# Optimization experiments

Hardware: AMD Instinct MI355X
Metric: run time of the kernel (lower is better)

The kernel has to match this reference:

```python
import jax, jax.numpy as jnp
import numpy as np

LATENT = 128
K_SUBTREES = 64      # children of the root '&&'
DEPTH = 11           # perfect binary subtree depth -> 2**11 = 2048 leaves each
N_NODES = 50000      # program-graph node embedding rows
N_TOKENS = 32        # len(LIST_PREDICATES) + len(LIST_OP)


def setup_inputs() -> dict:
    key = jax.random.key(0)
    ks = jax.random.split(key, 16)
    L = LATENT
    s = 0.08  # keep tanh/sigmoid out of saturation, like trained weights
    return {
        "node_embedding": jax.random.normal(ks[0], (N_NODES, L), jnp.float32) * 0.5,
        "init_embedding": jax.random.normal(ks[1], (1, L), jnp.float32) * 0.5,
        "char_embedding": jax.random.normal(ks[2], (N_TOKENS, L), jnp.float32) * 0.5,
        # stacked gate weights, y = x @ W + b
        # W_child order: ilh, irh, lflh, lfrh, rflh, rfrh, ulh, urh
        "W_child": jax.random.normal(ks[3], (8, L, L), jnp.float32) * s,
        "b_child": jax.random.normal(ks[4], (8, L), jnp.float32) * s,
        # W_x order: ix, fx, ux
        "W_x": jax.random.normal(ks[5], (3, L, L), jnp.float32) * s,
        "b_x": jax.random.normal(ks[6], (3, L), jnp.float32) * s,
        # W_leaf order: cx, ox
        "W_leaf": jax.random.normal(ks[7], (2, L, L), jnp.float32) * s,
        "b_leaf": jax.random.normal(ks[8], (2, L), jnp.float32) * s,
        # W_and order: and_transform_c, and_transform_h
        "W_and": jax.random.normal(ks[9], (2, L, L), jnp.float32) * s,
        "b_and": jax.random.normal(ks[10], (2, L), jnp.float32) * s,
        "W_oend": jax.random.normal(ks[11], (3 * L, L), jnp.float32) * s,
        "b_oend": jax.random.normal(ks[12], (L,), jnp.float32) * s,
        "leaf_idx": jax.random.randint(ks[13], (K_SUBTREES, 2 ** DEPTH), 0, N_NODES, jnp.int32),
        "op_idx": jax.random.randint(ks[14], (K_SUBTREES, 2 ** DEPTH - 1), 0, N_TOKENS, jnp.int32),
    }


def reference(node_embedding, init_embedding, char_embedding,
              W_child, b_child, W_x, b_x, W_leaf, b_leaf,
              W_and, b_and, W_oend, b_oend, leaf_idx, op_idx):
    n_leaves = leaf_idx.shape[1]
    depth = int(np.log2(n_leaves))

    # --- leaves: c = cx(x); h = sigmoid(ox(x)) * tanh(c) ---
    x = node_embedding[leaf_idx]                      # [K, M, L]
    c = x @ W_leaf[0] + b_leaf[0]
    h = jax.nn.sigmoid(x @ W_leaf[1] + b_leaf[1]) * jnp.tanh(c)

    # --- internal binary Tree-LSTM cells, level by level (bottom-up) ---
    start = 0
    for d in range(depth):
        m = n_leaves >> (d + 1)                       # nodes at this level
        xe = char_embedding[op_idx[:, start:start + m]]  # [K, m, L]
        start += m
        lc, rc = c[:, 0::2], c[:, 1::2]
        lh, rh = h[:, 0::2], h[:, 1::2]
        # fused gate projections: [3|4, K, m, L]
        gx = jnp.einsum('kml,gld->gkmd', xe, W_x) + b_x[:, None, None, :]
        gl = jnp.einsum('kml,gld->gkmd', lh, W_child[0::2]) + b_child[0::2, None, None, :]
        gr = jnp.einsum('kml,gld->gkmd', rh, W_child[1::2]) + b_child[1::2, None, None, :]
        i = jax.nn.sigmoid(gx[0] + gl[0] + gr[0])          # ix + ilh + irh
        lf = jax.nn.sigmoid(gx[1] + gl[1] + gr[1])         # fx + lflh + lfrh
        rf = jax.nn.sigmoid(gx[1] + gl[2] + gr[2])         # fx + rflh + rfrh
        u = jnp.tanh(gx[2] + gl[3] + gr[3])                # ux + ulh + urh
        c = i * u + lf * lc + rf * rc
        h = jnp.tanh(c)

    # --- root '&&': transform, min-pool over children, output gate ---
    c2 = c[:, 0] @ W_and[0] + b_and[0]                 # [K, L]
    h2 = h[:, 0] @ W_and[1] + b_and[1]
    cmin = jnp.min(c2, axis=0, keepdims=True)          # [1, L]
    hmin = jnp.min(h2, axis=0, keepdims=True)
    s = jnp.concatenate([init_embedding, cmin, hmin], axis=1)  # [1, 3L]
    return jnp.tanh(s @ W_oend + b_oend)
```

## Files before the change

kernel.cpp:

```cpp
#include <hip/hip_runtime.h>

#define NNODES 50000

typedef _Float16 half8 __attribute__((ext_vector_type(8)));
typedef float f32x4 __attribute__((ext_vector_type(4)));

__device__ __forceinline__ float sigm(float x)   { return 1.f / (1.f + __expf(-x)); }
__device__ __forceinline__ float tanh_f(float x) { float e = __expf(2.f * x); return 1.f - 2.f / (e + 1.f); }

__global__ __launch_bounds__(256) void k_prep(const float* __restrict__ Wc,
                                              const float* __restrict__ Wl,
                                              const float* __restrict__ ce,
                                              const float* __restrict__ Wx,
                                              const float* __restrict__ bx,
                                              const float* __restrict__ bc,
                                              _Float16* __restrict__ WpT,
                                              _Float16* __restrict__ WlT) {
    int b = blockIdx.x;
    if (b < 512) {
        int i = b * 256 + threadIdx.x;
        int c = i >> 8, k = i & 255;
        int g = c >> 7, d = c & 127;
        float v = (k < 128) ? Wc[(2 * g) * 16384 + k * 128 + d]
                            : Wc[(2 * g + 1) * 16384 + (k - 128) * 128 + d];
        WpT[c * 288 + k] = (_Float16)v;
    } else if (b < 640) {
        int i = (b - 512) * 256 + threadIdx.x;
        int c = i >> 7, k = i & 127;
        WlT[i] = (_Float16)Wl[(c >> 7) * 16384 + k * 128 + (c & 127)];
    } else {
        int i = (b - 640) * 256 + threadIdx.x;
        int tt = i >> 9, c = i & 511;
        int g = c >> 7, d = c & 127;
        int gx = (g == 0) ? 0 : ((g == 3) ? 2 : 1);
        float acc = bx[gx * 128 + d] + bc[(2 * g) * 128 + d] + bc[(2 * g + 1) * 128 + d];
        const float* x = ce + tt * 128;
        const float* w = Wx + gx * 16384 + d;
        for (int l = 0; l < 128; ++l) acc += x[l] * w[l * 128];
        WpT[c * 288 + 256 + tt] = (_Float16)acc;
    }
}

__global__ __launch_bounds__(256) void k_prep_nodes(const float* __restrict__ ne,
                                                    const _Float16* __restrict__ WlT,
                                                    const float* __restrict__ bl,
                                                    _Float16* __restrict__ c_tab,
                                                    _Float16* __restrict__ h_tab) {
    const int t = threadIdx.x;
    const int w = t >> 6, l = t & 63;
    const int lr = l & 15, lq = l >> 4;
    const int nb = blockIdx.x * 32;

    int arow[2];
#pragma unroll
    for (int rt = 0; rt < 2; ++rt) {
        int r = nb + rt * 16 + lr;
        arow[rt] = (r < NNODES) ? r : (NNODES - 1);
    }

    f32x4 acc[2][2][2];
#pragma unroll
    for (int rt = 0; rt < 2; ++rt)
#pragma unroll
        for (int g = 0; g < 2; ++g)
#pragma unroll
            for (int ti = 0; ti < 2; ++ti) acc[rt][g][ti] = (f32x4)0.f;

#pragma unroll
    for (int kk = 0; kk < 4; ++kk) {
        half8 af[2];
#pragma unroll
        for (int rt = 0; rt < 2; ++rt) {
            const float* src = ne + (size_t)arow[rt] * 128 + kk * 32 + lq * 8;
            float4 f0 = *(const float4*)src;
            float4 f1 = *(const float4*)(src + 4);
            half8 v;
            v[0] = (_Float16)f0.x; v[1] = (_Float16)f0.y; v[2] = (_Float16)f0.z; v[3] = (_Float16)f0.w;
            v[4] = (_Float16)f1.x; v[5] = (_Float16)f1.y; v[6] = (_Float16)f1.z; v[7] = (_Float16)f1.w;
            af[rt] = v;
        }
#pragma unroll
        for (int g = 0; g < 2; ++g)
#pragma unroll
            for (int ti = 0; ti < 2; ++ti) {
                int col = g * 128 + w * 32 + ti * 16 + lr;
                half8 bb = *(const half8*)(WlT + col * 128 + kk * 32 + lq * 8);
#pragma unroll
                for (int rt = 0; rt < 2; ++rt)
                    acc[rt][g][ti] = __builtin_amdgcn_mfma_f32_16x16x32_f16(af[rt], bb, acc[rt][g][ti], 0, 0, 0);
            }
    }

#pragma unroll
    for (int rt = 0; rt < 2; ++rt)
#pragma unroll
        for (int j = 0; j < 4; ++j) {
            int r = nb + rt * 16 + lq * 4 + j;
            if (r < NNODES) {
#pragma unroll
                for (int ti = 0; ti < 2; ++ti) {
                    int d = w * 32 + ti * 16 + lr;
                    float cc = acc[rt][0][ti][j] + bl[d];
                    float hp = acc[rt][1][ti][j] + bl[128 + d];
                    c_tab[(size_t)r * 128 + d] = (_Float16)cc;
                    h_tab[(size_t)r * 128 + d] = (_Float16)(sigm(hp) * tanh_f(cc));
                }
            }
        }
}


__device__ __forceinline__ void lo_quarter(int qb,
                                           const _Float16* __restrict__ c_tab,
                                           const _Float16* __restrict__ h_tab,
                                           const int* s_leaf, const int* s_op,
                                           const half8 (&B)[9][4],
                                           _Float16* hA, _Float16* cA,
                                           int lq, int lr, int dcol) {
    _Float16 lcv[4], rcv[4];
#pragma unroll
    for (int j = 0; j < 4; ++j) {
        int p = qb + lq * 4 + j;
        lcv[j] = c_tab[(size_t)s_leaf[2 * p] * 128 + dcol];
        rcv[j] = c_tab[(size_t)s_leaf[2 * p + 1] * 128 + dcol];
    }
    const int pg = qb + lr;
    const int gl = s_leaf[2 * pg], gr = s_leaf[2 * pg + 1];
    const int opv = s_op[pg];
    half8 af[8];
#pragma unroll
    for (int kk = 0; kk < 8; ++kk) {
        int row = (kk < 4) ? gl : gr;
        af[kk] = *(const half8*)(h_tab + (size_t)row * 128 + (kk & 3) * 32 + lq * 8);
    }
    f32x4 acc[4];
#pragma unroll
    for (int g = 0; g < 4; ++g) acc[g] = (f32x4)0.f;
#pragma unroll
    for (int kk = 0; kk < 9; ++kk) {
        half8 a;
        if (kk < 8) a = af[kk];
        else {
#pragma unroll
            for (int i = 0; i < 8; ++i)
                a[i] = (_Float16)((lq * 8 + i) == opv ? 1.f : 0.f);
        }
#pragma unroll
        for (int g = 0; g < 4; ++g)
            acc[g] = __builtin_amdgcn_mfma_f32_16x16x32_f16(a, B[kk][g], acc[g], 0, 0, 0);
    }
#pragma unroll
    for (int j = 0; j < 4; ++j) {
        int p = qb + lq * 4 + j;
        float vi = acc[0][j], vl = acc[1][j], vr = acc[2][j], vu = acc[3][j];
        float cc = sigm(vi) * tanh_f(vu) + sigm(vl) * (float)lcv[j] + sigm(vr) * (float)rcv[j];
        cA[p * 132 + dcol] = (_Float16)cc;
        hA[p * 128 + (dcol ^ ((p & 15) << 3))] = (_Float16)tanh_f(cc);
    }
}

template <int NP, bool G3OUT>
__device__ __forceinline__ void lds_pass(int pass0, int opoff,
                                         const _Float16* hS, const _Float16* cS,
                                         _Float16* hD, _Float16* cD,
                                         float* __restrict__ gc, _Float16* __restrict__ gh,
                                         int growbase,
                                         const int* s_op, const half8 (&B)[9][4],
                                         int lq, int lr, int dcol) {
    const int pidx = pass0 + ((NP >= 16) ? lr : (lr & (NP - 1)));
    const int opv = s_op[opoff + pidx];
    f32x4 acc[4];
#pragma unroll
    for (int g = 0; g < 4; ++g) acc[g] = (f32x4)0.f;
#pragma unroll
    for (int kk = 0; kk < 9; ++kk) {
        half8 a;
        if (kk < 8) {
            int side = kk >> 2, ko = (kk & 3) * 32 + lq * 8;
            int child = 2 * pidx + side;
            a = *(const half8*)(hS + child * 128 + (ko ^ ((child & 15) << 3)));
        } else {
#pragma unroll
            for (int i = 0; i < 8; ++i)
                a[i] = (_Float16)((lq * 8 + i) == opv ? 1.f : 0.f);
        }
#pragma unroll
        for (int g = 0; g < 4; ++g)
            acc[g] = __builtin_amdgcn_mfma_f32_16x16x32_f16(a, B[kk][g], acc[g], 0, 0, 0);
    }
#pragma unroll
    for (int j = 0; j < 4; ++j) {
        int p = pass0 + lq * 4 + j;
        if (p < pass0 + NP) {
            float vi = acc[0][j], vl = acc[1][j], vr = acc[2][j], vu = acc[3][j];
            float lc = (float)cS[(2 * p) * 132 + dcol];
            float rc = (float)cS[(2 * p + 1) * 132 + dcol];
            float cc = sigm(vi) * tanh_f(vu) + sigm(vl) * lc + sigm(vr) * rc;
            if constexpr (G3OUT) {
                gc[(size_t)(growbase + p) * 128 + dcol] = cc;
                gh[(size_t)(growbase + p) * 128 + dcol] = (_Float16)tanh_f(cc);
            } else {
                cD[p * 132 + dcol] = (_Float16)cc;
                hD[p * 128 + (dcol ^ ((p & 15) << 3))] = (_Float16)tanh_f(cc);
            }
        }
    }
}

__global__ __launch_bounds__(512, 2) void k_lo(const _Float16* __restrict__ c_tab,
                                               const _Float16* __restrict__ h_tab,
                                               const int* __restrict__ leaf_idx,
                                               const int* __restrict__ op_idx,
                                               const _Float16* __restrict__ WpT,
                                               float* __restrict__ g3c,
                                               _Float16* __restrict__ g3h) {
    __shared__ int s_leaf[128];
    __shared__ int s_op[120];
    __shared__ _Float16 hA[64 * 128], cA[64 * 132];
    __shared__ _Float16 hB[32 * 128], cB[32 * 132];

    const int t = threadIdx.x;
    const int w = t >> 6, l = t & 63, lr = l & 15, lq = l >> 4;
    const int ks = blockIdx.x >> 4, seg = blockIdx.x & 15;
    const int dcol = w * 16 + lr;

    if (t < 128) s_leaf[t] = leaf_idx[ks * 2048 + seg * 128 + t];
    else if (t < 192) s_op[t - 128] = op_idx[ks * 2047 + seg * 64 + (t - 128)];
    else if (t < 224) s_op[64 + t - 192] = op_idx[ks * 2047 + 1024 + seg * 32 + (t - 192)];
    else if (t < 240) s_op[96 + t - 224] = op_idx[ks * 2047 + 1536 + seg * 16 + (t - 224)];
    else if (t < 248) s_op[112 + t - 240] = op_idx[ks * 2047 + 1792 + seg * 8 + (t - 240)];
    __syncthreads();

    half8 B[9][4];
#pragma unroll
    for (int kk = 0; kk < 9; ++kk)
#pragma unroll
        for (int g = 0; g < 4; ++g)
            B[kk][g] = *(const half8*)(WpT + (g * 128 + dcol) * 288 + kk * 32 + lq * 8);

    lo_quarter( 0, c_tab, h_tab, s_leaf, s_op, B, hA, cA, lq, lr, dcol);
    lo_quarter(16, c_tab, h_tab, s_leaf, s_op, B, hA, cA, lq, lr, dcol);
    lo_quarter(32, c_tab, h_tab, s_leaf, s_op, B, hA, cA, lq, lr, dcol);
    lo_quarter(48, c_tab, h_tab, s_leaf, s_op, B, hA, cA, lq, lr, dcol);
    __syncthreads();

    lds_pass<16, false>( 0, 64, hA, cA, hB, cB, nullptr, nullptr, 0, s_op, B, lq, lr, dcol);
    lds_pass<16, false>(16, 64, hA, cA, hB, cB, nullptr, nullptr, 0, s_op, B, lq, lr, dcol);
    __syncthreads();

    lds_pass<16, false>(0, 96, hB, cB, hA, cA, nullptr, nullptr, 0, s_op, B, lq, lr, dcol);
    __syncthreads();

    lds_pass<8, true>(0, 112, hA, cA, nullptr, nullptr, g3c, g3h, blockIdx.x * 8,
                      s_op, B, lq, lr, dcol);
}

template <int NRT, bool GSRC>
__device__ __forceinline__ void tail_pass(int np, int pass0, int opoff,
                                          const _Float16* hS, const _Float16* cS,
                                          const _Float16* __restrict__ gh,
                                          const float* __restrict__ gc, int rowbase,
                                          _Float16* hD, _Float16* cD,
                                          const half8 (&B)[9][4],
                                          const int* s_op, int w, int lq, int lr) {
    f32x4 acc[NRT][4];
#pragma unroll
    for (int rt = 0; rt < NRT; ++rt)
#pragma unroll
        for (int g = 0; g < 4; ++g) acc[rt][g] = (f32x4)0.f;

    int pidx[NRT], opv[NRT];
#pragma unroll
    for (int rt = 0; rt < NRT; ++rt) {
        int p = pass0 + rt * 16 + lr;
        pidx[rt] = (p < np) ? p : (np - 1);
        opv[rt] = s_op[opoff + pidx[rt]];
    }

#pragma unroll
    for (int kk = 0; kk < 9; ++kk) {
        half8 a[NRT];
        if (kk < 8) {
            int side = kk >> 2, ko = (kk & 3) * 32 + lq * 8;
#pragma unroll
            for (int rt = 0; rt < NRT; ++rt) {
                int child = 2 * pidx[rt] + side;
                if constexpr (GSRC)
                    a[rt] = *(const half8*)(gh + (size_t)(rowbase + child) * 128 + ko);
                else
                    a[rt] = *(const half8*)(hS + child * 128 + (ko ^ ((child & 15) << 3)));
            }
        } else {
#pragma unroll
            for (int rt = 0; rt < NRT; ++rt)
#pragma unroll
                for (int i = 0; i < 8; ++i)
                    a[rt][i] = (_Float16)((lq * 8 + i) == opv[rt] ? 1.f : 0.f);
        }
#pragma unroll
        for (int rt = 0; rt < NRT; ++rt)
#pragma unroll
            for (int g = 0; g < 4; ++g)
                acc[rt][g] = __builtin_amdgcn_mfma_f32_16x16x32_f16(a[rt], B[kk][g], acc[rt][g], 0, 0, 0);
    }

    const int d = w * 16 + lr;
#pragma unroll
    for (int rt = 0; rt < NRT; ++rt)
#pragma unroll
        for (int j = 0; j < 4; ++j) {
            int p = pass0 + rt * 16 + lq * 4 + j;
            if (p < np) {
                float vi = acc[rt][0][j], vl = acc[rt][1][j];
                float vr = acc[rt][2][j], vu = acc[rt][3][j];
                float lc, rc;
                if constexpr (GSRC) {
                    lc = gc[(size_t)(rowbase + 2 * p) * 128 + d];
                    rc = gc[(size_t)(rowbase + 2 * p + 1) * 128 + d];
                } else {
                    lc = (float)cS[(2 * p) * 132 + d];
                    rc = (float)cS[(2 * p + 1) * 132 + d];
                }
                float cc = sigm(vi) * tanh_f(vu) + sigm(vl) * lc + sigm(vr) * rc;
                cD[p * 132 + d] = (_Float16)cc;
                hD[p * 128 + (d ^ ((p & 15) << 3))] = (_Float16)tanh_f(cc);
            }
        }
}

__global__ __launch_bounds__(512, 2) void k_tail4(const float* __restrict__ g3c,
                                                  const _Float16* __restrict__ g3h,
                                                  const int* __restrict__ op_idx,
                                                  const _Float16* __restrict__ WpT,
                                                  const float* __restrict__ Wa,
                                                  const float* __restrict__ ba,
                                                  float* __restrict__ c2,
                                                  float* __restrict__ h2) {
    __shared__ int s_op[128];
    __shared__ _Float16 hA[64 * 128], cA[64 * 132];
    __shared__ _Float16 hB[32 * 128], cB[32 * 132];
    const int t = threadIdx.x, w = t >> 6, l = t & 63, lr = l & 15, lq = l >> 4;
    const int tree = blockIdx.x;
    const int rb = tree * 128;

    if (t < 127) s_op[t] = op_idx[tree * 2047 + 1920 + t];
    __syncthreads();

    half8 B[9][4];
#pragma unroll
    for (int kk = 0; kk < 9; ++kk)
#pragma unroll
        for (int g = 0; g < 4; ++g)
            B[kk][g] = *(const half8*)(WpT + (g * 128 + w * 16 + lr) * 288 + kk * 32 + lq * 8);

    tail_pass<2, true>(64,  0, 0, nullptr, nullptr, g3h, g3c, rb, hA, cA, B, s_op, w, lq, lr);
    tail_pass<2, true>(64, 32, 0, nullptr, nullptr, g3h, g3c, rb, hA, cA, B, s_op, w, lq, lr);
    __syncthreads();
    tail_pass<2, false>(32, 0, 64, hA, cA, nullptr, nullptr, 0, hB, cB, B, s_op, w, lq, lr);
    __syncthreads();
    tail_pass<1, false>(16, 0,  96, hB, cB, nullptr, nullptr, 0, hA, cA, B, s_op, w, lq, lr);
    __syncthreads();
    tail_pass<1, false>( 8, 0, 112, hA, cA, nullptr, nullptr, 0, hB, cB, B, s_op, w, lq, lr);
    __syncthreads();
    tail_pass<1, false>( 4, 0, 120, hB, cB, nullptr, nullptr, 0, hA, cA, B, s_op, w, lq, lr);
    __syncthreads();
    tail_pass<1, false>( 2, 0, 124, hA, cA, nullptr, nullptr, 0, hB, cB, B, s_op, w, lq, lr);
    __syncthreads();
    tail_pass<1, false>( 1, 0, 126, hB, cB, nullptr, nullptr, 0, hA, cA, B, s_op, w, lq, lr);
    __syncthreads();

    if (t < 256) {
        int dd = t & 127;
        if (t < 128) {
            float a = ba[dd];
            for (int ll = 0; ll < 128; ++ll) a += (float)cA[ll] * Wa[ll * 128 + dd];
            c2[tree * 128 + dd] = a;
        } else {
            float a = ba[128 + dd];
            for (int ll = 0; ll < 128; ++ll) a += (float)hA[ll] * Wa[16384 + ll * 128 + dd];
            h2[tree * 128 + dd] = a;
        }
    }
}

__global__ __launch_bounds__(128) void k_final(const float* __restrict__ c2,
                                               const float* __restrict__ h2,
                                               const float* __restrict__ init_e,
                                               const float* __restrict__ Wo,
                                               const float* __restrict__ bo,
                                               float* __restrict__ out) {
    __shared__ float s[384];
    const int d = threadIdx.x;
    float cm = c2[d], hm = h2[d];
    for (int k = 1; k < 64; ++k) {
        cm = fminf(cm, c2[k * 128 + d]);
        hm = fminf(hm, h2[k * 128 + d]);
    }
    s[d] = init_e[d];
    s[128 + d] = cm;
    s[256 + d] = hm;
    __syncthreads();
    float a = bo[d];
    for (int l = 0; l < 384; ++l) a += s[l] * Wo[l * 128 + d];
    out[d] = tanhf(a);
}

extern "C" void kernel_launch(void* const* d_in, const int* in_sizes, int n_in,
                              void* d_out, int out_size, void* d_ws, size_t ws_size,
                              hipStream_t stream) {
    const float* node_emb = (const float*)d_in[0];
    const float* init_emb = (const float*)d_in[1];
    const float* char_emb = (const float*)d_in[2];
    const float* W_child  = (const float*)d_in[3];
    const float* b_child  = (const float*)d_in[4];
    const float* W_x      = (const float*)d_in[5];
    const float* b_x      = (const float*)d_in[6];
    const float* W_leaf   = (const float*)d_in[7];
    const float* b_leaf   = (const float*)d_in[8];
    const float* W_and    = (const float*)d_in[9];
    const float* b_and    = (const float*)d_in[10];
    const float* W_oend   = (const float*)d_in[11];
    const float* b_oend   = (const float*)d_in[12];
    const int* leaf_idx   = (const int*)d_in[13];
    const int* op_idx     = (const int*)d_in[14];
    float* out = (float*)d_out;
    (void)in_sizes; (void)n_in; (void)out_size; (void)ws_size;

    char* p = (char*)d_ws;
    auto carve = [&](size_t bytes) { char* r = p; p += (bytes + 255) & ~255ull; return r; };
    _Float16* WpT   = (_Float16*)carve((size_t)512 * 288 * 2);
    _Float16* WlT   = (_Float16*)carve((size_t)256 * 128 * 2);
    _Float16* c_tab = (_Float16*)carve((size_t)NNODES * 128 * 2);
    _Float16* h_tab = (_Float16*)carve((size_t)NNODES * 128 * 2);
    float*    g3c   = (float*)carve((size_t)8192 * 128 * 4);
    _Float16* g3h   = (_Float16*)carve((size_t)8192 * 128 * 2);
    float*    c2    = (float*)carve(64 * 128 * 4);
    float*    h2    = (float*)carve(64 * 128 * 4);

    k_prep      <<<704, 256, 0, stream>>>(W_child, W_leaf, char_emb, W_x, b_x, b_child, WpT, WlT);
    k_prep_nodes<<<(NNODES + 31) / 32, 256, 0, stream>>>(node_emb, WlT, b_leaf, c_tab, h_tab);

    k_lo   <<<1024, 512, 0, stream>>>(c_tab, h_tab, leaf_idx, op_idx, WpT, g3c, g3h);
    k_tail4<<<  64, 512, 0, stream>>>(g3c, g3h, op_idx, WpT, W_and, b_and, c2, h2);
    k_final<<<1, 128, 0, stream>>>(c2, h2, init_emb, W_oend, b_oend, out);
}
```

Baseline: 185.7 us.

## Software-pipeline leaf gathers with MFMA and precompute one-hot op rows in LDS

```diff
diff --git a/kernel.cpp b/kernel.cpp
--- a/kernel.cpp
+++ b/kernel.cpp
@@ -110,65 +110,113 @@
 }
 
 
-__device__ __forceinline__ void lo_quarter(int qb,
-                                           const _Float16* __restrict__ c_tab,
-                                           const _Float16* __restrict__ h_tab,
-                                           const int* s_leaf, const int* s_op,
-                                           const half8 (&B)[9][4],
-                                           _Float16* hA, _Float16* cA,
-                                           int lq, int lr, int dcol) {
-    _Float16 lcv[4], rcv[4];
+struct LoQ { half8 af[8]; _Float16 lcv[4], rcv[4]; };
+
+__device__ __forceinline__ void lo_gather(int qb,
+                                          const _Float16* __restrict__ c_tab,
+                                          const _Float16* __restrict__ h_tab,
+                                          const int* s_leaf,
+                                          int lq, int lr, int dcol, LoQ& s) {
 #pragma unroll
     for (int j = 0; j < 4; ++j) {
         int p = qb + lq * 4 + j;
-        lcv[j] = c_tab[(size_t)s_leaf[2 * p] * 128 + dcol];
-        rcv[j] = c_tab[(size_t)s_leaf[2 * p + 1] * 128 + dcol];
+        s.lcv[j] = c_tab[(size_t)s_leaf[2 * p] * 128 + dcol];
+        s.rcv[j] = c_tab[(size_t)s_leaf[2 * p + 1] * 128 + dcol];
     }
     const int pg = qb + lr;
     const int gl = s_leaf[2 * pg], gr = s_leaf[2 * pg + 1];
-    const int opv = s_op[pg];
-    half8 af[8];
 #pragma unroll
     for (int kk = 0; kk < 8; ++kk) {
         int row = (kk < 4) ? gl : gr;
-        af[kk] = *(const half8*)(h_tab + (size_t)row * 128 + (kk & 3) * 32 + lq * 8);
-    }
-    f32x4 acc[4];
+        s.af[kk] = *(const half8*)(h_tab + (size_t)row * 128 + (kk & 3) * 32 + lq * 8);
+    }
+}
+
+__device__ __forceinline__ void lo_mfma(const LoQ& s, int qb, const _Float16* s_oh,
+                                        const half8 (&B)[9][4], int lq, int lr,
+                                        f32x4 (&acc)[4]) {
 #pragma unroll
     for (int g = 0; g < 4; ++g) acc[g] = (f32x4)0.f;
 #pragma unroll
     for (int kk = 0; kk < 9; ++kk) {
-        half8 a;
-        if (kk < 8) a = af[kk];
-        else {
-#pragma unroll
-            for (int i = 0; i < 8; ++i)
-                a[i] = (_Float16)((lq * 8 + i) == opv ? 1.f : 0.f);
-        }
+        half8 a = (kk < 8) ? s.af[kk]
+                           : *(const half8*)(s_oh + (qb + lr) * 36 + lq * 8);
 #pragma unroll
         for (int g = 0; g < 4; ++g)
             acc[g] = __builtin_amdgcn_mfma_f32_16x16x32_f16(a, B[kk][g], acc[g], 0, 0, 0);
     }
+}
+
+__device__ __forceinline__ void lo_epi(const f32x4 (&acc)[4], const LoQ& s, int qb,
+                                       _Float16* hA, _Float16* cA, int lq, int dcol) {
 #pragma unroll
     for (int j = 0; j < 4; ++j) {
         int p = qb + lq * 4 + j;
-        float vi = acc[0][j], vl = acc[1][j], vr = acc[2][j], vu = acc[3][j];
-        float cc = sigm(vi) * tanh_f(vu) + sigm(vl) * (float)lcv[j] + sigm(vr) * (float)rcv[j];
+        float cc = sigm(acc[0][j]) * tanh_f(acc[3][j])
+                 + sigm(acc[1][j]) * (float)s.lcv[j]
+                 + sigm(acc[2][j]) * (float)s.rcv[j];
         cA[p * 132 + dcol] = (_Float16)cc;
         hA[p * 128 + (dcol ^ ((p & 15) << 3))] = (_Float16)tanh_f(cc);
     }
 }
 
+__device__ __forceinline__ void lds_pass2(int opoff,
+                                          const _Float16* hS, const _Float16* cS,
+                                          _Float16* hD, _Float16* cD,
+                                          const _Float16* s_oh,
+                                          const half8 (&B)[9][4],
+                                          int lq, int lr, int dcol) {
+    f32x4 acc[2][4];
+#pragma unroll
+    for (int rt = 0; rt < 2; ++rt)
+#pragma unroll
+        for (int g = 0; g < 4; ++g) acc[rt][g] = (f32x4)0.f;
+
+#pragma unroll
+    for (int kk = 0; kk < 9; ++kk) {
+        half8 a[2];
+        if (kk < 8) {
+            int side = kk >> 2, ko = (kk & 3) * 32 + lq * 8;
+#pragma unroll
+            for (int rt = 0; rt < 2; ++rt) {
+                int child = 2 * (rt * 16 + lr) + side;
+                a[rt] = *(const half8*)(hS + child * 128 + (ko ^ ((child & 15) << 3)));
+            }
+        } else {
+            a[0] = *(const half8*)(s_oh + (opoff + lr) * 36 + lq * 8);
+            a[1] = *(const half8*)(s_oh + (opoff + 16 + lr) * 36 + lq * 8);
+        }
+#pragma unroll
+        for (int rt = 0; rt < 2; ++rt)
+#pragma unroll
+            for (int g = 0; g < 4; ++g)
+                acc[rt][g] = __builtin_amdgcn_mfma_f32_16x16x32_f16(a[rt], B[kk][g], acc[rt][g], 0, 0, 0);
+    }
+
+#pragma unroll
+    for (int rt = 0; rt < 2; ++rt)
+#pragma unroll
+        for (int j = 0; j < 4; ++j) {
+            int p = rt * 16 + lq * 4 + j;
+            float vi = acc[rt][0][j], vl = acc[rt][1][j];
+            float vr = acc[rt][2][j], vu = acc[rt][3][j];
+            float lc = (float)cS[(2 * p) * 132 + dcol];
+            float rc = (float)cS[(2 * p + 1) * 132 + dcol];
+            float cc = sigm(vi) * tanh_f(vu) + sigm(vl) * lc + sigm(vr) * rc;
+            cD[p * 132 + dcol] = (_Float16)cc;
+            hD[p * 128 + (dcol ^ ((p & 15) << 3))] = (_Float16)tanh_f(cc);
+        }
+}
+
 template <int NP, bool G3OUT>
-__device__ __forceinline__ void lds_pass(int pass0, int opoff,
+__device__ __forceinline__ void lds_pass(int opoff,
                                          const _Float16* hS, const _Float16* cS,
                                          _Float16* hD, _Float16* cD,
                                          float* __restrict__ gc, _Float16* __restrict__ gh,
                                          int growbase,
-                                         const int* s_op, const half8 (&B)[9][4],
+                                         const _Float16* s_oh, const half8 (&B)[9][4],
                                          int lq, int lr, int dcol) {
-    const int pidx = pass0 + ((NP >= 16) ? lr : (lr & (NP - 1)));
-    const int opv = s_op[opoff + pidx];
+    const int pidx = (NP >= 16) ? lr : (lr & (NP - 1));
     f32x4 acc[4];
 #pragma unroll
     for (int g = 0; g < 4; ++g) acc[g] = (f32x4)0.f;
@@ -180,9 +228,7 @@
             int child = 2 * pidx + side;
             a = *(const half8*)(hS + child * 128 + (ko ^ ((child & 15) << 3)));
         } else {
-#pragma unroll
-            for (int i = 0; i < 8; ++i)
-                a[i] = (_Float16)((lq * 8 + i) == opv ? 1.f : 0.f);
+            a = *(const half8*)(s_oh + (opoff + pidx) * 36 + lq * 8);
         }
 #pragma unroll
         for (int g = 0; g < 4; ++g)
@@ -190,8 +236,8 @@
     }
 #pragma unroll
     for (int j = 0; j < 4; ++j) {
-        int p = pass0 + lq * 4 + j;
-        if (p < pass0 + NP) {
+        int p = lq * 4 + j;
+        if (p < NP) {
             float vi = acc[0][j], vl = acc[1][j], vr = acc[2][j], vu = acc[3][j];
             float lc = (float)cS[(2 * p) * 132 + dcol];
             float rc = (float)cS[(2 * p + 1) * 132 + dcol];
@@ -216,6 +262,7 @@
                                                _Float16* __restrict__ g3h) {
     __shared__ int s_leaf[128];
     __shared__ int s_op[120];
+    __shared__ _Float16 s_oh[120 * 36];
     __shared__ _Float16 hA[64 * 128], cA[64 * 132];
     __shared__ _Float16 hB[32 * 128], cB[32 * 132];
 
@@ -229,7 +276,6 @@
     else if (t < 224) s_op[64 + t - 192] = op_idx[ks * 2047 + 1024 + seg * 32 + (t - 192)];
     else if (t < 240) s_op[96 + t - 224] = op_idx[ks * 2047 + 1536 + seg * 16 + (t - 224)];
     else if (t < 248) s_op[112 + t - 240] = op_idx[ks * 2047 + 1792 + seg * 8 + (t - 240)];
-    __syncthreads();
 
     half8 B[9][4];
 #pragma unroll
@@ -238,21 +284,41 @@
         for (int g = 0; g < 4; ++g)
             B[kk][g] = *(const half8*)(WpT + (g * 128 + dcol) * 288 + kk * 32 + lq * 8);
 
-    lo_quarter( 0, c_tab, h_tab, s_leaf, s_op, B, hA, cA, lq, lr, dcol);
-    lo_quarter(16, c_tab, h_tab, s_leaf, s_op, B, hA, cA, lq, lr, dcol);
-    lo_quarter(32, c_tab, h_tab, s_leaf, s_op, B, hA, cA, lq, lr, dcol);
-    lo_quarter(48, c_tab, h_tab, s_leaf, s_op, B, hA, cA, lq, lr, dcol);
-    __syncthreads();
-
-    lds_pass<16, false>( 0, 64, hA, cA, hB, cB, nullptr, nullptr, 0, s_op, B, lq, lr, dcol);
-    lds_pass<16, false>(16, 64, hA, cA, hB, cB, nullptr, nullptr, 0, s_op, B, lq, lr, dcol);
-    __syncthreads();
-
-    lds_pass<16, false>(0, 96, hB, cB, hA, cA, nullptr, nullptr, 0, s_op, B, lq, lr, dcol);
-    __syncthreads();
-
-    lds_pass<8, true>(0, 112, hA, cA, nullptr, nullptr, g3c, g3h, blockIdx.x * 8,
-                      s_op, B, lq, lr, dcol);
+    __syncthreads();
+    for (int i = t; i < 120 * 32; i += 512) {
+        int p = i >> 5, k = i & 31;
+        s_oh[p * 36 + k] = (_Float16)((k == s_op[p]) ? 1.f : 0.f);
+    }
+    __syncthreads();
+
+    LoQ q0, q1;
+    f32x4 acc[4];
+    lo_gather(0, c_tab, h_tab, s_leaf, lq, lr, dcol, q0);
+
+    lo_mfma(q0, 0, s_oh, B, lq, lr, acc);
+    lo_gather(16, c_tab, h_tab, s_leaf, lq, lr, dcol, q1);
+    lo_epi(acc, q0, 0, hA, cA, lq, dcol);
+
+    lo_mfma(q1, 16, s_oh, B, lq, lr, acc);
+    lo_gather(32, c_tab, h_tab, s_leaf, lq, lr, dcol, q0);
+    lo_epi(acc, q1, 16, hA, cA, lq, dcol);
+
+    lo_mfma(q0, 32, s_oh, B, lq, lr, acc);
+    lo_gather(48, c_tab, h_tab, s_leaf, lq, lr, dcol, q1);
+    lo_epi(acc, q0, 32, hA, cA, lq, dcol);
+
+    lo_mfma(q1, 48, s_oh, B, lq, lr, acc);
+    lo_epi(acc, q1, 48, hA, cA, lq, dcol);
+    __syncthreads();
+
+    lds_pass2(64, hA, cA, hB, cB, s_oh, B, lq, lr, dcol);
+    __syncthreads();
+
+    lds_pass<16, false>(96, hB, cB, hA, cA, nullptr, nullptr, 0, s_oh, B, lq, lr, dcol);
+    __syncthreads();
+
+    lds_pass<8, true>(112, hA, cA, nullptr, nullptr, g3c, g3h, blockIdx.x * 8,
+                      s_oh, B, lq, lr, dcol);
 }
 
 template <int NRT, bool GSRC>
@@ -261,20 +327,20 @@
                                           const _Float16* __restrict__ gh,
                                           const float* __restrict__ gc, int rowbase,
                                           _Float16* hD, _Float16* cD,
+                                          const _Float16* s_oh,
                                           const half8 (&B)[9][4],
-                                          const int* s_op, int w, int lq, int lr) {
+                                          const int* , int w, int lq, int lr) {
     f32x4 acc[NRT][4];
 #pragma unroll
     for (int rt = 0; rt < NRT; ++rt)
 #pragma unroll
         for (int g = 0; g < 4; ++g) acc[rt][g] = (f32x4)0.f;
 
-    int pidx[NRT], opv[NRT];
+    int pidx[NRT];
 #pragma unroll
     for (int rt = 0; rt < NRT; ++rt) {
         int p = pass0 + rt * 16 + lr;
         pidx[rt] = (p < np) ? p : (np - 1);
-        opv[rt] = s_op[opoff + pidx[rt]];
     }
 
 #pragma unroll
@@ -293,9 +359,7 @@
         } else {
 #pragma unroll
             for (int rt = 0; rt < NRT; ++rt)
-#pragma unroll
-                for (int i = 0; i < 8; ++i)
-                    a[rt][i] = (_Float16)((lq * 8 + i) == opv[rt] ? 1.f : 0.f);
+                a[rt] = *(const half8*)(s_oh + (opoff + pidx[rt]) * 36 + lq * 8);
         }
 #pragma unroll
         for (int rt = 0; rt < NRT; ++rt)
@@ -337,6 +401,7 @@
                                                   float* __restrict__ c2,
                                                   float* __restrict__ h2) {
     __shared__ int s_op[128];
+    __shared__ _Float16 s_oh[127 * 36];
     __shared__ _Float16 hA[64 * 128], cA[64 * 132];
     __shared__ _Float16 hB[32 * 128], cB[32 * 132];
     const int t = threadIdx.x, w = t >> 6, l = t & 63, lr = l & 15, lq = l >> 4;
@@ -344,7 +409,6 @@
     const int rb = tree * 128;
 
     if (t < 127) s_op[t] = op_idx[tree * 2047 + 1920 + t];
-    __syncthreads();
 
     half8 B[9][4];
 #pragma unroll
@@ -353,20 +417,27 @@
         for (int g = 0; g < 4; ++g)
             B[kk][g] = *(const half8*)(WpT + (g * 128 + w * 16 + lr) * 288 + kk * 32 + lq * 8);
 
-    tail_pass<2, true>(64,  0, 0, nullptr, nullptr, g3h, g3c, rb, hA, cA, B, s_op, w, lq, lr);
-    tail_pass<2, true>(64, 32, 0, nullptr, nullptr, g3h, g3c, rb, hA, cA, B, s_op, w, lq, lr);
-    __syncthreads();
-    tail_pass<2, false>(32, 0, 64, hA, cA, nullptr, nullptr, 0, hB, cB, B, s_op, w, lq, lr);
-    __syncthreads();
-    tail_pass<1, false>(16, 0,  96, hB, cB, nullptr, nullptr, 0, hA, cA, B, s_op, w, lq, lr);
-    __syncthreads();
-    tail_pass<1, false>( 8, 0, 112, hA, cA, nullptr, nullptr, 0, hB, cB, B, s_op, w, lq, lr);
-    __syncthreads();
-    tail_pass<1, false>( 4, 0, 120, hB, cB, nullptr, nullptr, 0, hA, cA, B, s_op, w, lq, lr);
-    __syncthreads();
-    tail_pass<1, false>( 2, 0, 124, hA, cA, nullptr, nullptr, 0, hB, cB, B, s_op, w, lq, lr);
-    __syncthreads();
-    tail_pass<1, false>( 1, 0, 126, hB, cB, nullptr, nullptr, 0, hA, cA, B, s_op, w, lq, lr);
+    __syncthreads();
+    for (int i = t; i < 127 * 32; i += 512) {
+        int p = i >> 5, k = i & 31;
+        s_oh[p * 36 + k] = (_Float16)((k == s_op[p]) ? 1.f : 0.f);
+    }
+    __syncthreads();
+
+    tail_pass<2, true>(64,  0, 0, nullptr, nullptr, g3h, g3c, rb, hA, cA, s_oh, B, s_op, w, lq, lr);
+    tail_pass<2, true>(64, 32, 0, nullptr, nullptr, g3h, g3c, rb, hA, cA, s_oh, B, s_op, w, lq, lr);
+    __syncthreads();
+    tail_pass<2, false>(32, 0, 64, hA, cA, nullptr, nullptr, 0, hB, cB, s_oh, B, s_op, w, lq, lr);
+    __syncthreads();
+    tail_pass<1, false>(16, 0,  96, hB, cB, nullptr, nullptr, 0, hA, cA, s_oh, B, s_op, w, lq, lr);
+    __syncthreads();
+    tail_pass<1, false>( 8, 0, 112, hA, cA, nullptr, nullptr, 0, hB, cB, s_oh, B, s_op, w, lq, lr);
+    __syncthreads();
+    tail_pass<1, false>( 4, 0, 120, hB, cB, nullptr, nullptr, 0, hA, cA, s_oh, B, s_op, w, lq, lr);
+    __syncthreads();
+    tail_pass<1, false>( 2, 0, 124, hA, cA, nullptr, nullptr, 0, hB, cB, s_oh, B, s_op, w, lq, lr);
+    __syncthreads();
+    tail_pass<1, false>( 1, 0, 126, hB, cB, nullptr, nullptr, 0, hA, cA, s_oh, B, s_op, w, lq, lr);
     __syncthreads();
 
     if (t < 256) {
```

Result: no change. 185.3 us (-0.2%).
